# Kernel optimization log

Hardware: AMD Instinct MI355X
Metric: run time of the kernel (lower is better)

The kernel has to match this reference:

```python
import jax, jax.numpy as jnp
import numpy as np

NUM_LAYERS = 9
HIDDEN = 3


def _param_indices(hidden, num_layers):
    # Mirrors DistributionFreeModel.calculate_parameter_indices
    offset = 3 + (num_layers - 2) * (hidden + 2)
    idx = [((0 * hidden, 1 * hidden), (1 * hidden, 2 * hidden), (2 * hidden, 3 * hidden))]
    for o in range(3, offset, hidden + 2):
        idx.append((
            (o * hidden, (o + hidden) * hidden),
            ((o + hidden) * hidden, (o + hidden + 1) * hidden),
            ((o + hidden + 1) * hidden, (o + hidden + 2) * hidden),
        ))
    idx.append(((offset * hidden, (offset + 1) * hidden),
                ((offset + 1) * hidden, (offset + 1) * hidden + 1),
                None))
    return idx


def _cdf(inputs, parameters, hidden=HIDDEN, num_layers=NUM_LAYERS):
    # inputs: [B, F]; parameters: [F, P]
    out = inputs[..., None]  # [B, F, 1]
    for li, (wi, bi, si) in enumerate(_param_indices(hidden, num_layers)):
        w = parameters[..., wi[0]:wi[1]]
        b = parameters[..., bi[0]:bi[1]]
        if li == 0:
            w = w.reshape(w.shape[:-1] + (hidden, 1))
        elif li == num_layers - 1:
            w = w.reshape(w.shape[:-1] + (1, hidden))
        else:
            w = w.reshape(w.shape[:-1] + (hidden, hidden))
        w = jax.nn.softplus(w)
        # per-feature tiny matmul, broadcast over batch: [B,F,f] x [F,d,f] -> [B,F,d]
        out = jnp.einsum('...f,...df->...d', out, w) + b
        if si is not None:
            s = jnp.tanh(parameters[..., si[0]:si[1]])
            out = out + s * jnp.tanh(out)
    return jax.nn.sigmoid(out)[..., 0]  # squeeze last dim -> [B, F]


def setup_inputs() -> dict:
    key = jax.random.key(0)
    k1, k2 = jax.random.split(key)
    B, F = 32768, 512
    P = (NUM_LAYERS - 2) * HIDDEN ** 2 + 2 * NUM_LAYERS * HIDDEN + 1  # 118
    inputs = jax.random.normal(k1, (B, F), dtype=jnp.float32)
    parameters = jax.random.normal(k2, (F, P), dtype=jnp.float32)
    return {"inputs": inputs, "parameters": parameters}


def reference(inputs, parameters):
    return _cdf(inputs, parameters)
```

## Files before the change

### kernel.cpp

```cpp
#include <hip/hip_runtime.h>
#include <math.h>

#define NF 512
#define NP 118
#define NPPAD 126
#define FT 16
#define ROWS 8
#define BLOCK_ROWS 128
#define TBL_N 2048
#define WS_NEED ((size_t)(NPPAD * NF + 2 * TBL_N) * sizeof(float))

typedef float v2f __attribute__((ext_vector_type(2)));

__device__ __forceinline__ v2f f_PP(v2f a, v2f b, v2f c) {
    v2f d; asm("v_pk_fma_f32 %0, %1, %2, %3" : "=v"(d) : "v"(a), "v"(b), "v"(c)); return d;
}
__device__ __forceinline__ v2f f_LP(v2f a, v2f b, v2f c) {
    v2f d; asm("v_pk_fma_f32 %0, %1, %2, %3 op_sel_hi:[1,0,1]" : "=v"(d) : "v"(a), "v"(b), "v"(c)); return d;
}
__device__ __forceinline__ v2f f_HP(v2f a, v2f b, v2f c) {
    v2f d; asm("v_pk_fma_f32 %0, %1, %2, %3 op_sel:[0,1,0] op_sel_hi:[1,1,1]" : "=v"(d) : "v"(a), "v"(b), "v"(c)); return d;
}
__device__ __forceinline__ v2f f_LH(v2f a, v2f b, v2f c) {
    v2f d; asm("v_pk_fma_f32 %0, %1, %2, %3 op_sel:[0,0,1] op_sel_hi:[1,0,1]" : "=v"(d) : "v"(a), "v"(b), "v"(c)); return d;
}
__device__ __forceinline__ v2f f_HL(v2f a, v2f b, v2f c) {
    v2f d; asm("v_pk_fma_f32 %0, %1, %2, %3 op_sel:[0,1,0] op_sel_hi:[1,1,0]" : "=v"(d) : "v"(a), "v"(b), "v"(c)); return d;
}

__device__ __forceinline__ v2f tanh_pair(v2f x, const v2f* __restrict__ tbl,
                                         v2f K128, v2f K1024) {
    v2f xi = f_PP(x, K128, K1024);
    float q0 = __builtin_amdgcn_fmed3f(xi.x, 0.0f, 2047.0f);
    float q1 = __builtin_amdgcn_fmed3f(xi.y, 0.0f, 2047.0f);
    v2f sc0 = tbl[(int)q0];
    v2f sc1 = tbl[(int)q1];
    v2f r;
    r.x = fmaf(x.x, sc0.x, sc0.y);
    r.y = fmaf(x.y, sc1.x, sc1.y);
    return r;
}

__device__ __forceinline__ float transform_one(float v, int j) {
    int cls;
    if (j < 3) cls = 0;
    else if (j < 6) cls = 1;
    else if (j < 9) cls = 2;
    else if (j < 114) { int k = (j - 9) % 15; cls = (k < 9) ? 0 : ((k < 12) ? 1 : 2); }
    else if (j < 117) cls = 0;
    else cls = 1;
    if (cls == 0) return fmaxf(v, 0.0f) + log1pf(expf(-fabsf(v)));
    if (cls == 2) return tanhf(v);
    return v;
}

__device__ __forceinline__ bool map_padded(int jp, int* j) {
    if (jp < 9) { *j = jp; return true; }
    if (jp == 9) return false;
    if (jp < 122) {
        int k = (jp - 10) & 15, li = (jp - 10) >> 4;
        if (k == 15) return false;
        *j = 9 + 15 * li + k;
        return true;
    }
    *j = 114 + (jp - 122);
    return true;
}

__device__ __forceinline__ float transform_padded(const float* __restrict__ prow, int jp) {
    int j;
    if (!map_padded(jp, &j)) return 0.0f;
    float v = transform_one(prow[j], j);
    if (jp >= 122) v *= 0.5f;
    return v;
}

__device__ __forceinline__ void tbl_entry(int b, float* s, float* c) {
    float xl = (float)b * (1.0f / 128.0f) - (1024.5f / 128.0f);
    float xr = xl + (1.0f / 128.0f);
    float t0 = tanhf(xl), t1 = tanhf(xr);
    float sl = (t1 - t0) * 128.0f;
    *s = sl;
    *c = fmaf(-sl, xl, t0);
}

__global__ void xform_kernel(const float* __restrict__ p, float* __restrict__ t) {
    int idx = blockIdx.x * 256 + threadIdx.x;
    if (idx < NPPAD * NF) {
        int jp = idx / NF, f = idx - jp * NF;
        t[idx] = transform_padded(p + f * NP, jp);
    } else if (idx < NPPAD * NF + TBL_N) {
        int bin = idx - NPPAD * NF;
        float s, c;
        tbl_entry(bin, &s, &c);
        t[NPPAD * NF + 2 * bin]     = s;
        t[NPPAD * NF + 2 * bin + 1] = c;
    }
}

template <bool FUSE_XFORM>
__global__ __launch_bounds__(256, 6)
void cdf_kernel(const float* __restrict__ x, const float* __restrict__ prm,
                float* __restrict__ out) {
    __shared__ float ldsp[NPPAD * FT];
    __shared__ v2f   tblv[TBL_N];
    const int tid = threadIdx.x;
    const int fi  = tid & (FT - 1);
    const int rg  = tid >> 4;
    const int f0  = blockIdx.x * FT;
    const int b0  = blockIdx.y * BLOCK_ROWS + rg * ROWS;
    const int f   = f0 + fi;

    if constexpr (FUSE_XFORM) {
        for (int idx = tid; idx < NPPAD * FT; idx += 256) {
            int jp = idx >> 4, fl = idx & (FT - 1);
            ldsp[(jp >> 1) * (2 * FT) + fl * 2 + (jp & 1)] =
                transform_padded(prm + (f0 + fl) * NP, jp);
        }
        float* tf = (float*)tblv;
        for (int bin = tid; bin < TBL_N; bin += 256) {
            float s, c; tbl_entry(bin, &s, &c);
            tf[2 * bin] = s; tf[2 * bin + 1] = c;
        }
    } else {
        for (int idx = tid; idx < NPPAD * FT; idx += 256) {
            int jp = idx >> 4, fl = idx & (FT - 1);
            ldsp[(jp >> 1) * (2 * FT) + fl * 2 + (jp & 1)] = prm[jp * NF + f0 + fl];
        }
        float* tf = (float*)tblv;
        const float* tw = prm + NPPAD * NF;
        for (int idx = tid; idx < 2 * TBL_N; idx += 256)
            tf[idx] = tw[idx];
    }

    v2f xin[4];
#pragma unroll
    for (int r = 0; r < 4; ++r) {
        xin[r].x = x[(b0 + 2 * r)     * NF + f];
        xin[r].y = x[(b0 + 2 * r + 1) * NF + f];
    }

    __syncthreads();

    const v2f K128  = {128.0f, 128.0f};
    const v2f K1024 = {1024.5f, 1024.5f};
    const v2f Khalf = {0.5f, 0.5f};

    const float* Pp = ldsp + fi * 2;
#define PRMV(JP) (*reinterpret_cast<const v2f*>(Pp + (JP) * FT))

    v2f h0[4], h1[4], h2[4];
    {
        v2f q0 = PRMV(0), q1 = PRMV(2), q2 = PRMV(4), q3 = PRMV(6), q4 = PRMV(8);
#pragma unroll
        for (int r = 0; r < 4; ++r) {
            v2f a0 = f_LH(xin[r], q0, q1);
            v2f a1 = f_HL(xin[r], q0, q2);
            v2f a2 = f_LH(xin[r], q1, q2);
            v2f T0 = tanh_pair(a0, tblv, K128, K1024);
            v2f T1 = tanh_pair(a1, tblv, K128, K1024);
            v2f T2 = tanh_pair(a2, tblv, K128, K1024);
            h0[r] = f_LP(T0, q3, a0);
            h1[r] = f_HP(T1, q3, a1);
            h2[r] = f_LP(T2, q4, a2);
        }
    }
#pragma unroll
    for (int li = 1; li < 8; ++li) {
        const int bp = 10 + 16 * (li - 1);
        v2f q0 = PRMV(bp + 0), q1 = PRMV(bp + 2), q2 = PRMV(bp + 4), q3 = PRMV(bp + 6);
        v2f q4 = PRMV(bp + 8), q5 = PRMV(bp + 10), q6 = PRMV(bp + 12), q7 = PRMV(bp + 14);
#pragma unroll
        for (int r = 0; r < 4; ++r) {
            v2f t0 = f_LH(h0[r], q0, q4);
            t0     = f_HP(h1[r], q0, t0);
            v2f a0 = f_LP(h2[r], q1, t0);
            v2f t1 = f_HL(h0[r], q1, q5);
            t1     = f_LP(h1[r], q2, t1);
            v2f a1 = f_HP(h2[r], q2, t1);
            v2f t2 = f_LH(h0[r], q3, q5);
            t2     = f_HP(h1[r], q3, t2);
            v2f a2 = f_LP(h2[r], q4, t2);
            v2f T0 = tanh_pair(a0, tblv, K128, K1024);
            v2f T1 = tanh_pair(a1, tblv, K128, K1024);
            v2f T2 = tanh_pair(a2, tblv, K128, K1024);
            h0[r] = f_LP(T0, q6, a0);
            h1[r] = f_HP(T1, q6, a1);
            h2[r] = f_LP(T2, q7, a2);
        }
    }
    {
        v2f q8 = PRMV(122), q9 = PRMV(124);
#pragma unroll
        for (int r = 0; r < 4; ++r) {
            v2f a = f_LH(h0[r], q8, q9);
            a     = f_HP(h1[r], q8, a);
            a     = f_LP(h2[r], q9, a);
            v2f T = tanh_pair(a, tblv, K128, K1024);
            v2f o = f_PP(T, Khalf, Khalf);
            out[(b0 + 2 * r)     * NF + f] = o.x;
            out[(b0 + 2 * r + 1) * NF + f] = o.y;
        }
    }
#undef PRMV
}

extern "C" void kernel_launch(void* const* d_in, const int* in_sizes, int n_in,
                              void* d_out, int out_size, void* d_ws, size_t ws_size,
                              hipStream_t stream) {
    const float* x = (const float*)d_in[0];
    const float* p = (const float*)d_in[1];
    float* out = (float*)d_out;

    const int B = in_sizes[0] / NF;
    dim3 grid(NF / FT, B / BLOCK_ROWS);
    dim3 block(256);

    if (ws_size >= WS_NEED) {
        float* t = (float*)d_ws;
        int total = NPPAD * NF + TBL_N;
        xform_kernel<<<(total + 255) / 256, 256, 0, stream>>>(p, t);
        cdf_kernel<false><<<grid, block, 0, stream>>>(x, t, out);
    } else {
        cdf_kernel<true><<<grid, block, 0, stream>>>(x, p, out);
    }
}
```

Before: 104.9 us.

## Software-pipeline tanh table lookups across row pairs and widen feature tile

The per-layer loop over four row pairs is restructured so that the LDS table gathers for one pair are issued before the previous pair's results are consumed. This overlaps LDS lookup latency with FMA work. The feature tile grows from 16 to 32 and rows per block drop from 128 to 64, and the launch-bounds occupancy hint is lowered from 6 to 4 to leave registers for the extra in-flight gather results. The cost is higher register pressure and lower occupancy, and the parameter tile in LDS doubles.

```diff
diff --git a/kernel.cpp b/kernel.cpp
--- a/kernel.cpp
+++ b/kernel.cpp
@@ -4,9 +4,9 @@
 #define NF 512
 #define NP 118
 #define NPPAD 126
-#define FT 16
+#define FT 32
 #define ROWS 8
-#define BLOCK_ROWS 128
+#define BLOCK_ROWS 64
 #define TBL_N 2048
 #define WS_NEED ((size_t)(NPPAD * NF + 2 * TBL_N) * sizeof(float))
 
@@ -26,19 +26,6 @@
 }
 __device__ __forceinline__ v2f f_HL(v2f a, v2f b, v2f c) {
     v2f d; asm("v_pk_fma_f32 %0, %1, %2, %3 op_sel:[0,1,0] op_sel_hi:[1,1,0]" : "=v"(d) : "v"(a), "v"(b), "v"(c)); return d;
-}
-
-__device__ __forceinline__ v2f tanh_pair(v2f x, const v2f* __restrict__ tbl,
-                                         v2f K128, v2f K1024) {
-    v2f xi = f_PP(x, K128, K1024);
-    float q0 = __builtin_amdgcn_fmed3f(xi.x, 0.0f, 2047.0f);
-    float q1 = __builtin_amdgcn_fmed3f(xi.y, 0.0f, 2047.0f);
-    v2f sc0 = tbl[(int)q0];
-    v2f sc1 = tbl[(int)q1];
-    v2f r;
-    r.x = fmaf(x.x, sc0.x, sc0.y);
-    r.y = fmaf(x.y, sc1.x, sc1.y);
-    return r;
 }
 
 __device__ __forceinline__ float transform_one(float v, int j) {
@@ -99,21 +86,21 @@
 }
 
 template <bool FUSE_XFORM>
-__global__ __launch_bounds__(256, 6)
+__global__ __launch_bounds__(256, 4)
 void cdf_kernel(const float* __restrict__ x, const float* __restrict__ prm,
                 float* __restrict__ out) {
     __shared__ float ldsp[NPPAD * FT];
     __shared__ v2f   tblv[TBL_N];
     const int tid = threadIdx.x;
     const int fi  = tid & (FT - 1);
-    const int rg  = tid >> 4;
+    const int rg  = tid >> 5;
     const int f0  = blockIdx.x * FT;
     const int b0  = blockIdx.y * BLOCK_ROWS + rg * ROWS;
     const int f   = f0 + fi;
 
     if constexpr (FUSE_XFORM) {
         for (int idx = tid; idx < NPPAD * FT; idx += 256) {
-            int jp = idx >> 4, fl = idx & (FT - 1);
+            int jp = idx >> 5, fl = idx & (FT - 1);
             ldsp[(jp >> 1) * (2 * FT) + fl * 2 + (jp & 1)] =
                 transform_padded(prm + (f0 + fl) * NP, jp);
         }
@@ -124,7 +111,7 @@
         }
     } else {
         for (int idx = tid; idx < NPPAD * FT; idx += 256) {
-            int jp = idx >> 4, fl = idx & (FT - 1);
+            int jp = idx >> 5, fl = idx & (FT - 1);
             ldsp[(jp >> 1) * (2 * FT) + fl * 2 + (jp & 1)] = prm[jp * NF + f0 + fl];
         }
         float* tf = (float*)tblv;
@@ -142,67 +129,100 @@
 
     __syncthreads();
 
-    const v2f K128  = {128.0f, 128.0f};
-    const v2f K1024 = {1024.5f, 1024.5f};
+    const v2f K128 = {128.0f, 128.0f};
+    const v2f KIdx = {1024.5f, 1024.5f};
     const v2f Khalf = {0.5f, 0.5f};
 
     const float* Pp = ldsp + fi * 2;
 #define PRMV(JP) (*reinterpret_cast<const v2f*>(Pp + (JP) * FT))
 
+#define IDXG(a, Glo, Ghi) {                                              \
+        v2f xi_ = f_PP((a), K128, KIdx);                                 \
+        int i0_ = (int)__builtin_amdgcn_fmed3f(xi_.x, 0.0f, 2047.0f);    \
+        int i1_ = (int)__builtin_amdgcn_fmed3f(xi_.y, 0.0f, 2047.0f);    \
+        (Glo) = tblv[i0_]; (Ghi) = tblv[i1_]; }
+
+#define TCOMB(a, Glo, Ghi) ({ v2f t_;                                    \
+        t_.x = fmaf((a).x, (Glo).x, (Glo).y);                            \
+        t_.y = fmaf((a).y, (Ghi).x, (Ghi).y); t_; })
+
     v2f h0[4], h1[4], h2[4];
+    v2f A0[4], A1[4], A2[4];
+    v2f G00[4], G01[4], G10[4], G11[4], G20[4], G21[4];
+
     {
         v2f q0 = PRMV(0), q1 = PRMV(2), q2 = PRMV(4), q3 = PRMV(6), q4 = PRMV(8);
-#pragma unroll
-        for (int r = 0; r < 4; ++r) {
-            v2f a0 = f_LH(xin[r], q0, q1);
-            v2f a1 = f_HL(xin[r], q0, q2);
-            v2f a2 = f_LH(xin[r], q1, q2);
-            v2f T0 = tanh_pair(a0, tblv, K128, K1024);
-            v2f T1 = tanh_pair(a1, tblv, K128, K1024);
-            v2f T2 = tanh_pair(a2, tblv, K128, K1024);
-            h0[r] = f_LP(T0, q3, a0);
-            h1[r] = f_HP(T1, q3, a1);
-            h2[r] = f_LP(T2, q4, a2);
-        }
-    }
+#define ISSUE_L0(p) {                                                    \
+        A0[p] = f_LH(xin[p], q0, q1);                                    \
+        A1[p] = f_HL(xin[p], q0, q2);                                    \
+        A2[p] = f_LH(xin[p], q1, q2);                                    \
+        IDXG(A0[p], G00[p], G01[p]);                                     \
+        IDXG(A1[p], G10[p], G11[p]);                                     \
+        IDXG(A2[p], G20[p], G21[p]); }
+#define CONSUME_L0(p) {                                                  \
+        v2f T0 = TCOMB(A0[p], G00[p], G01[p]);                           \
+        v2f T1 = TCOMB(A1[p], G10[p], G11[p]);                           \
+        v2f T2 = TCOMB(A2[p], G20[p], G21[p]);                           \
+        h0[p] = f_LP(T0, q3, A0[p]);                                     \
+        h1[p] = f_HP(T1, q3, A1[p]);                                     \
+        h2[p] = f_LP(T2, q4, A2[p]); }
+        ISSUE_L0(0); ISSUE_L0(1); CONSUME_L0(0);
+        ISSUE_L0(2); CONSUME_L0(1);
+        ISSUE_L0(3); CONSUME_L0(2); CONSUME_L0(3);
+#undef ISSUE_L0
+#undef CONSUME_L0
+    }
+
 #pragma unroll
     for (int li = 1; li < 8; ++li) {
         const int bp = 10 + 16 * (li - 1);
         v2f q0 = PRMV(bp + 0), q1 = PRMV(bp + 2), q2 = PRMV(bp + 4), q3 = PRMV(bp + 6);
         v2f q4 = PRMV(bp + 8), q5 = PRMV(bp + 10), q6 = PRMV(bp + 12), q7 = PRMV(bp + 14);
-#pragma unroll
-        for (int r = 0; r < 4; ++r) {
-            v2f t0 = f_LH(h0[r], q0, q4);
-            t0     = f_HP(h1[r], q0, t0);
-            v2f a0 = f_LP(h2[r], q1, t0);
-            v2f t1 = f_HL(h0[r], q1, q5);
-            t1     = f_LP(h1[r], q2, t1);
-            v2f a1 = f_HP(h2[r], q2, t1);
-            v2f t2 = f_LH(h0[r], q3, q5);
-            t2     = f_HP(h1[r], q3, t2);
-            v2f a2 = f_LP(h2[r], q4, t2);
-            v2f T0 = tanh_pair(a0, tblv, K128, K1024);
-            v2f T1 = tanh_pair(a1, tblv, K128, K1024);
-            v2f T2 = tanh_pair(a2, tblv, K128, K1024);
-            h0[r] = f_LP(T0, q6, a0);
-            h1[r] = f_HP(T1, q6, a1);
-            h2[r] = f_LP(T2, q7, a2);
-        }
-    }
+#define ISSUE_MID(p) {                                                   \
+        v2f t0 = f_LH(h0[p], q0, q4); t0 = f_HP(h1[p], q0, t0);          \
+        A0[p] = f_LP(h2[p], q1, t0);                                     \
+        v2f t1 = f_HL(h0[p], q1, q5); t1 = f_LP(h1[p], q2, t1);          \
+        A1[p] = f_HP(h2[p], q2, t1);                                     \
+        v2f t2 = f_LH(h0[p], q3, q5); t2 = f_HP(h1[p], q3, t2);          \
+        A2[p] = f_LP(h2[p], q4, t2);                                     \
+        IDXG(A0[p], G00[p], G01[p]);                                     \
+        IDXG(A1[p], G10[p], G11[p]);                                     \
+        IDXG(A2[p], G20[p], G21[p]); }
+#define CONSUME_MID(p) {                                                 \
+        v2f T0 = TCOMB(A0[p], G00[p], G01[p]);                           \
+        v2f T1 = TCOMB(A1[p], G10[p], G11[p]);                           \
+        v2f T2 = TCOMB(A2[p], G20[p], G21[p]);                           \
+        h0[p] = f_LP(T0, q6, A0[p]);                                     \
+        h1[p] = f_HP(T1, q6, A1[p]);                                     \
+        h2[p] = f_LP(T2, q7, A2[p]); }
+        ISSUE_MID(0); ISSUE_MID(1); CONSUME_MID(0);
+        ISSUE_MID(2); CONSUME_MID(1);
+        ISSUE_MID(3); CONSUME_MID(2); CONSUME_MID(3);
+#undef ISSUE_MID
+#undef CONSUME_MID
+    }
+
     {
         v2f q8 = PRMV(122), q9 = PRMV(124);
-#pragma unroll
-        for (int r = 0; r < 4; ++r) {
-            v2f a = f_LH(h0[r], q8, q9);
-            a     = f_HP(h1[r], q8, a);
-            a     = f_LP(h2[r], q9, a);
-            v2f T = tanh_pair(a, tblv, K128, K1024);
-            v2f o = f_PP(T, Khalf, Khalf);
-            out[(b0 + 2 * r)     * NF + f] = o.x;
-            out[(b0 + 2 * r + 1) * NF + f] = o.y;
-        }
+#define ISSUE_FIN(p) {                                                   \
+        v2f a_ = f_LH(h0[p], q8, q9);                                    \
+        a_     = f_HP(h1[p], q8, a_);                                    \
+        A0[p]  = f_LP(h2[p], q9, a_);                                    \
+        IDXG(A0[p], G00[p], G01[p]); }
+#define CONSUME_FIN(p) {                                                 \
+        v2f T = TCOMB(A0[p], G00[p], G01[p]);                            \
+        v2f o = f_PP(T, Khalf, Khalf);                                   \
+        out[(b0 + 2 * (p))     * NF + f] = o.x;                          \
+        out[(b0 + 2 * (p) + 1) * NF + f] = o.y; }
+        ISSUE_FIN(0); ISSUE_FIN(1); CONSUME_FIN(0);
+        ISSUE_FIN(2); CONSUME_FIN(1);
+        ISSUE_FIN(3); CONSUME_FIN(2); CONSUME_FIN(3);
+#undef ISSUE_FIN
+#undef CONSUME_FIN
     }
 #undef PRMV
+#undef IDXG
+#undef TCOMB
 }
 
 extern "C" void kernel_launch(void* const* d_in, const int* in_sizes, int n_in,
```

After: 113.7 us. +8.4%, slower.
